# Kernel tuning notes

Measured on AMD Instinct MI355X. Metric: run time of the kernel, lower is better.

Reference implementation:

```python
import jax, jax.numpy as jnp
import numpy as np

NUM_BINS = 20
TEMPERATURE = 0.1
EPS = 1e-8


def setup_inputs() -> dict:
    key = jax.random.key(0)
    k1, k2 = jax.random.split(key)
    shape = (32, 1, 1024, 1024)  # B, C, H, W segmentation-style probability maps
    preds = jax.random.uniform(k1, shape, dtype=jnp.float32)
    targets = jax.random.uniform(k2, shape, dtype=jnp.float32)
    return {"preds": preds, "targets": targets}


def reference(preds, targets):
    p = preds.reshape(-1)
    t = targets.reshape(-1)
    centers = jnp.linspace(0.0, 1.0, NUM_BINS, dtype=p.dtype)

    def per_bin(c):
        # Gaussian soft-assignment weights for this bin center
        w = jnp.exp(-(p - c) ** 2 / TEMPERATURE)
        w_sum = w.sum()
        e = (w * p).sum() / (w_sum + EPS)  # weighted mean confidence
        o = (w * t).sum() / (w_sum + EPS)  # weighted mean accuracy
        # torch code skips bins with zero total weight
        return jnp.where(w_sum == 0.0, jnp.zeros_like(e), jnp.abs(e - o))

    # lax.map loops sequentially over the 20 bin centers so we never
    # materialize a [NUM_BINS, N] weight matrix.
    contribs = jax.lax.map(per_bin, centers)
    return contribs.sum() / NUM_BINS
```

## Files before the change

kernel.cpp:

```cpp
#include <hip/hip_runtime.h>
#include <math.h>

#define NUM_BINS 20
#define NACC     (3 * NUM_BINS)
#define BLOCK    256
#define NBLK_MAX 2048

__device__ __host__ constexpr float K1f() { return (float)(-1.0 / (0.1 * 0.6931471805599453)); }
__device__ __host__ constexpr float K2f() { return (float)( 2.0 / (1.9 * 0.6931471805599453)); }

__global__ __launch_bounds__(BLOCK) void ace_partial(const float* __restrict__ p,
                                                     const float* __restrict__ t,
                                                     float* __restrict__ partials,
                                                     int n4) {
    const float K1 = K1f();
    const float K2 = K2f();

    float aW[NUM_BINS], aP[NUM_BINS], aT[NUM_BINS];
#pragma unroll
    for (int j = 0; j < NUM_BINS; ++j) { aW[j] = 0.f; aP[j] = 0.f; aT[j] = 0.f; }

    const float4* __restrict__ p4 = (const float4*)p;
    const float4* __restrict__ t4 = (const float4*)t;

    int tid    = blockIdx.x * BLOCK + threadIdx.x;
    int stride = gridDim.x * BLOCK;

    for (int i = tid; i < n4; i += stride) {
        float4 pv = p4[i];
        float4 tv = t4[i];

        float pe[4] = {pv.x, pv.y, pv.z, pv.w};
        float te[4] = {tv.x, tv.y, tv.z, tv.w};

#pragma unroll
        for (int e = 0; e < 4; ++e) {
            float pp = pe[e];
            float tt = te[e];
            float u  = __builtin_amdgcn_exp2f(K1 * pp * pp);
            float G  = __builtin_amdgcn_exp2f(K2 * pp);
            float g  = u;
#pragma unroll
            for (int j = 0; j < NUM_BINS; ++j) {
                aW[j] += g;
                aP[j]  = fmaf(g, pp, aP[j]);
                aT[j]  = fmaf(g, tt, aT[j]);
                g     *= G;
            }
        }
    }

#pragma unroll
    for (int j = 0; j < NUM_BINS; ++j) {
#pragma unroll
        for (int off = 32; off > 0; off >>= 1) {
            aW[j] += __shfl_down(aW[j], off, 64);
            aP[j] += __shfl_down(aP[j], off, 64);
            aT[j] += __shfl_down(aT[j], off, 64);
        }
    }

    __shared__ float red[BLOCK / 64][NACC];
    int wave = threadIdx.x >> 6;
    int lane = threadIdx.x & 63;
    if (lane == 0) {
#pragma unroll
        for (int j = 0; j < NUM_BINS; ++j) {
            red[wave][j]                = aW[j];
            red[wave][NUM_BINS + j]     = aP[j];
            red[wave][2 * NUM_BINS + j] = aT[j];
        }
    }
    __syncthreads();

    if (threadIdx.x < NACC) {
        float s = 0.f;
#pragma unroll
        for (int w = 0; w < BLOCK / 64; ++w) s += red[w][threadIdx.x];
        partials[blockIdx.x * NACC + threadIdx.x] = s;
    }
}

__global__ __launch_bounds__(1024) void ace_final(const float* __restrict__ partials,
                                                  float* __restrict__ out,
                                                  int nblk) {
    const float K1 = K1f();

    __shared__ float red[NACC][16];
    __shared__ float sums[NACC];
    int tid = threadIdx.x;

    if (tid < NACC * 16) {
        int j = tid >> 4;
        int k = tid & 15;
        float s = 0.f;
        for (int b = k; b < nblk; b += 16) s += partials[b * NACC + j];
        red[j][k] = s;
    }
    __syncthreads();

    if (tid < NACC) {
        float s = 0.f;
#pragma unroll
        for (int k = 0; k < 16; ++k) s += red[tid][k];
        sums[tid] = s;
    }
    __syncthreads();

    if (tid == 0) {
        float acc = 0.f;
        for (int j = 0; j < NUM_BINS; ++j) {
            float c    = (float)j / 19.0f;
            float A    = __builtin_amdgcn_exp2f(K1 * c * c);
            float wsum = A * sums[j];
            float denom = wsum + 1e-8f;
            float e    = (A * sums[NUM_BINS + j]) / denom;
            float o    = (A * sums[2 * NUM_BINS + j]) / denom;
            float contrib = (wsum == 0.0f) ? 0.0f : fabsf(e - o);
            acc += contrib;
        }
        out[0] = acc / (float)NUM_BINS;
    }
}

extern "C" void kernel_launch(void* const* d_in, const int* in_sizes, int n_in,
                              void* d_out, int out_size, void* d_ws, size_t ws_size,
                              hipStream_t stream) {
    const float* preds   = (const float*)d_in[0];
    const float* targets = (const float*)d_in[1];
    float* out           = (float*)d_out;
    float* partials      = (float*)d_ws;

    int n  = in_sizes[0];
    int n4 = n >> 2;

    int nblk = NBLK_MAX;
    size_t need = (size_t)nblk * NACC * sizeof(float);
    if (ws_size < need) {
        nblk = (int)(ws_size / (NACC * sizeof(float)));
        if (nblk > 1024) nblk = 1024;
        if (nblk < 1)    nblk = 1;
    }

    ace_partial<<<nblk, BLOCK, 0, stream>>>(preds, targets, partials, n4);
    ace_final<<<1, 1024, 0, stream>>>(partials, out, nblk);
}
```

Baseline: 318.5 us.

## Pack bin accumulators into float2 vectors and software-prefetch next input tile

Bin accumulators become pairs of 2-wide float vectors, and the geometric weight recurrence steps by G^2 across bin pairs. This is meant to let the compiler emit packed FMA/add/mul instructions (v_pk_fma_f32), roughly halving the VALU instruction count in the compute-bound inner loop. The grid-stride loop now prefetches the next float4 of preds/targets one iteration ahead, and the grid is cut to 1024 blocks with launch_bounds occupancy hint 4. The partials layout is transposed to bin-major for coalesced reads in the final kernel. The changes add register pressure and slightly change the floating-point rounding of the weight recurrence.

```diff
diff --git a/kernel.cpp b/kernel.cpp
--- a/kernel.cpp
+++ b/kernel.cpp
@@ -2,23 +2,30 @@
 #include <math.h>
 
 #define NUM_BINS 20
+#define NPAIR    (NUM_BINS / 2)
 #define NACC     (3 * NUM_BINS)
 #define BLOCK    256
-#define NBLK_MAX 2048
+#define NBLK     1024
+
+typedef float v2f __attribute__((ext_vector_type(2)));
 
 __device__ __host__ constexpr float K1f() { return (float)(-1.0 / (0.1 * 0.6931471805599453)); }
 __device__ __host__ constexpr float K2f() { return (float)( 2.0 / (1.9 * 0.6931471805599453)); }
 
-__global__ __launch_bounds__(BLOCK) void ace_partial(const float* __restrict__ p,
-                                                     const float* __restrict__ t,
-                                                     float* __restrict__ partials,
-                                                     int n4) {
+__global__ __launch_bounds__(BLOCK, 4) void ace_partial(const float* __restrict__ p,
+                                                        const float* __restrict__ t,
+                                                        float* __restrict__ partials,
+                                                        int n4, int nblk) {
     const float K1 = K1f();
     const float K2 = K2f();
 
-    float aW[NUM_BINS], aP[NUM_BINS], aT[NUM_BINS];
+    v2f aW2[NPAIR], aP2[NPAIR], aT2[NPAIR];
 #pragma unroll
-    for (int j = 0; j < NUM_BINS; ++j) { aW[j] = 0.f; aP[j] = 0.f; aT[j] = 0.f; }
+    for (int jp = 0; jp < NPAIR; ++jp) {
+        aW2[jp] = (v2f){0.f, 0.f};
+        aP2[jp] = (v2f){0.f, 0.f};
+        aT2[jp] = (v2f){0.f, 0.f};
+    }
 
     const float4* __restrict__ p4 = (const float4*)p;
     const float4* __restrict__ t4 = (const float4*)t;
@@ -26,37 +33,54 @@
     int tid    = blockIdx.x * BLOCK + threadIdx.x;
     int stride = gridDim.x * BLOCK;
 
-    for (int i = tid; i < n4; i += stride) {
+    int i = tid;
+    if (i < n4) {
         float4 pv = p4[i];
         float4 tv = t4[i];
+        for (;;) {
+            int inext = i + stride;
+            bool more = (inext < n4);
+            float4 pvn, tvn;
+            if (more) { pvn = p4[inext]; tvn = t4[inext]; }
 
-        float pe[4] = {pv.x, pv.y, pv.z, pv.w};
-        float te[4] = {tv.x, tv.y, tv.z, tv.w};
+            float pe[4] = {pv.x, pv.y, pv.z, pv.w};
+            float te[4] = {tv.x, tv.y, tv.z, tv.w};
 
 #pragma unroll
-        for (int e = 0; e < 4; ++e) {
-            float pp = pe[e];
-            float tt = te[e];
-            float u  = __builtin_amdgcn_exp2f(K1 * pp * pp);
-            float G  = __builtin_amdgcn_exp2f(K2 * pp);
-            float g  = u;
+            for (int e = 0; e < 4; ++e) {
+                float pp = pe[e];
+                float tt = te[e];
+                float u  = __builtin_amdgcn_exp2f(K1 * pp * pp);
+                float G  = __builtin_amdgcn_exp2f(K2 * pp);
+                float GG = G * G;
+                v2f g2;  g2.x = u;  g2.y = u * G;
+                v2f GG2 = (v2f){GG, GG};
+                v2f pp2 = (v2f){pp, pp};
+                v2f tt2 = (v2f){tt, tt};
 #pragma unroll
-            for (int j = 0; j < NUM_BINS; ++j) {
-                aW[j] += g;
-                aP[j]  = fmaf(g, pp, aP[j]);
-                aT[j]  = fmaf(g, tt, aT[j]);
-                g     *= G;
+                for (int jp = 0; jp < NPAIR; ++jp) {
+                    aW2[jp] += g2;
+                    aP2[jp]  = __builtin_elementwise_fma(g2, pp2, aP2[jp]);
+                    aT2[jp]  = __builtin_elementwise_fma(g2, tt2, aT2[jp]);
+                    g2      *= GG2;
+                }
             }
+
+            if (!more) break;
+            pv = pvn; tv = tvn; i = inext;
         }
     }
 
 #pragma unroll
-    for (int j = 0; j < NUM_BINS; ++j) {
+    for (int jp = 0; jp < NPAIR; ++jp) {
 #pragma unroll
         for (int off = 32; off > 0; off >>= 1) {
-            aW[j] += __shfl_down(aW[j], off, 64);
-            aP[j] += __shfl_down(aP[j], off, 64);
-            aT[j] += __shfl_down(aT[j], off, 64);
+            aW2[jp].x += __shfl_down(aW2[jp].x, off, 64);
+            aW2[jp].y += __shfl_down(aW2[jp].y, off, 64);
+            aP2[jp].x += __shfl_down(aP2[jp].x, off, 64);
+            aP2[jp].y += __shfl_down(aP2[jp].y, off, 64);
+            aT2[jp].x += __shfl_down(aT2[jp].x, off, 64);
+            aT2[jp].y += __shfl_down(aT2[jp].y, off, 64);
         }
     }
 
@@ -65,10 +89,13 @@
     int lane = threadIdx.x & 63;
     if (lane == 0) {
 #pragma unroll
-        for (int j = 0; j < NUM_BINS; ++j) {
-            red[wave][j]                = aW[j];
-            red[wave][NUM_BINS + j]     = aP[j];
-            red[wave][2 * NUM_BINS + j] = aT[j];
+        for (int jp = 0; jp < NPAIR; ++jp) {
+            red[wave][2 * jp]                    = aW2[jp].x;
+            red[wave][2 * jp + 1]                = aW2[jp].y;
+            red[wave][NUM_BINS + 2 * jp]         = aP2[jp].x;
+            red[wave][NUM_BINS + 2 * jp + 1]     = aP2[jp].y;
+            red[wave][2 * NUM_BINS + 2 * jp]     = aT2[jp].x;
+            red[wave][2 * NUM_BINS + 2 * jp + 1] = aT2[jp].y;
         }
     }
     __syncthreads();
@@ -77,7 +104,7 @@
         float s = 0.f;
 #pragma unroll
         for (int w = 0; w < BLOCK / 64; ++w) s += red[w][threadIdx.x];
-        partials[blockIdx.x * NACC + threadIdx.x] = s;
+        partials[threadIdx.x * nblk + blockIdx.x] = s;
     }
 }
 
@@ -94,7 +121,7 @@
         int j = tid >> 4;
         int k = tid & 15;
         float s = 0.f;
-        for (int b = k; b < nblk; b += 16) s += partials[b * NACC + j];
+        for (int b = k; b < nblk; b += 16) s += partials[j * nblk + b];
         red[j][k] = s;
     }
     __syncthreads();
@@ -134,14 +161,13 @@
     int n  = in_sizes[0];
     int n4 = n >> 2;
 
-    int nblk = NBLK_MAX;
+    int nblk = NBLK;
     size_t need = (size_t)nblk * NACC * sizeof(float);
     if (ws_size < need) {
         nblk = (int)(ws_size / (NACC * sizeof(float)));
-        if (nblk > 1024) nblk = 1024;
-        if (nblk < 1)    nblk = 1;
+        if (nblk < 1) nblk = 1;
     }
 
-    ace_partial<<<nblk, BLOCK, 0, stream>>>(preds, targets, partials, n4);
+    ace_partial<<<nblk, BLOCK, 0, stream>>>(preds, targets, partials, n4, nblk);
     ace_final<<<1, 1024, 0, stream>>>(partials, out, nblk);
 }
```

Measured after the change: 300.8 us. -5.5%, faster.
